# Optimization experiments

Hardware: AMD Instinct MI355X
Metric: run time of the kernel (lower is better)

## Reference

```python
import jax, jax.numpy as jnp
import numpy as np

N_NODES = 19385
N_EDGES = 1_200_000
GNN = 256
HID = 512
RANK = 512
NCLS = 3
NGENES = 6640
NBLK = 6
B = 256
EPS = 1e-5


def _ln(x, g, b):
    m = jnp.mean(x, axis=-1, keepdims=True)
    v = jnp.mean(jnp.square(x - m), axis=-1, keepdims=True)
    return (x - m) * jax.lax.rsqrt(v + EPS) * g + b


def setup_inputs() -> dict:
    key = jax.random.key(0)
    ks = iter(jax.random.split(key, 40))
    w = lambda shape, s=0.02: jax.random.normal(next(ks), shape, jnp.float32) * s
    inp = {
        'node_idx': jax.random.randint(next(ks), (B,), -1, N_NODES),  # -1 == OOV
        'edge_index': jax.random.randint(next(ks), (2, N_EDGES), 0, N_NODES),
        'edge_weight': jax.random.uniform(next(ks), (N_EDGES,), jnp.float32),
        'frozen_emb': jax.random.normal(next(ks), (N_NODES, GNN), jnp.float32),
        # trainable partial GNN (mps.6, mps.7, post_mp)
        'conv6_W': w((GNN, GNN)), 'conv6_b': jnp.zeros((GNN,)),
        'ln6_g': jnp.ones((GNN,)), 'ln6_b': jnp.zeros((GNN,)),
        'conv7_W': w((GNN, GNN)), 'conv7_b': jnp.zeros((GNN,)),
        'ln7_g': jnp.ones((GNN,)), 'ln7_b': jnp.zeros((GNN,)),
        'post_W': w((GNN, GNN)), 'post_b': jnp.zeros((GNN,)),
        # head
        'oov_emb': w((GNN,)),
        'in_ln_g': jnp.ones((GNN,)), 'in_ln_b': jnp.zeros((GNN,)),
        'proj_in_W': w((GNN, HID)), 'proj_in_b': jnp.zeros((HID,)),
        'rb_ln_g': jnp.ones((NBLK, HID)), 'rb_ln_b': jnp.zeros((NBLK, HID)),
        'rb_W1': w((NBLK, HID, 4 * HID)), 'rb_b1': jnp.zeros((NBLK, 4 * HID)),
        'rb_W2': w((NBLK, 4 * HID, HID)), 'rb_b2': jnp.zeros((NBLK, HID)),
        'out_ln_g': jnp.ones((HID,)), 'out_ln_b': jnp.zeros((HID,)),
        'bil_W': w((HID, NCLS * RANK)), 'bil_b': jnp.zeros((NCLS * RANK,)),
        'out_gene_emb': w((NGENES, RANK)),
    }
    return inp


def reference(node_idx, edge_index, edge_weight, frozen_emb,
              conv6_W, conv6_b, ln6_g, ln6_b,
              conv7_W, conv7_b, ln7_g, ln7_b,
              post_W, post_b,
              oov_emb, in_ln_g, in_ln_b, proj_in_W, proj_in_b,
              rb_ln_g, rb_ln_b, rb_W1, rb_b1, rb_W2, rb_b2,
              out_ln_g, out_ln_b, bil_W, bil_b, out_gene_emb):
    src, dst = edge_index[0], edge_index[1]

    def conv(x, W, b):
        # edge-weighted message passing: gather -> scale -> scatter-add -> linear
        msg = x[src] * edge_weight[:, None]              # [E, GNN]
        agg = jax.ops.segment_sum(msg, dst, num_segments=N_NODES)
        return agg @ W + b

    # trainable GNN layers (eval mode: dropout = identity)
    x = frozen_emb
    x = x + jax.nn.relu(_ln(conv(x, conv6_W, conv6_b), ln6_g, ln6_b))
    x = x + jax.nn.relu(_ln(conv(x, conv7_W, conv7_b), ln7_g, ln7_b))
    node_emb = x @ post_W + post_b                       # [N, GNN]

    # OOV-aware lookup
    in_f = (node_idx >= 0).astype(jnp.float32)[:, None]  # [B,1]
    gnn_emb = node_emb[jnp.clip(node_idx, 0, None)]      # [B, GNN]
    h = gnn_emb * in_f + oov_emb[None, :] * (1.0 - in_f)

    # MLP head
    h = _ln(h, in_ln_g, in_ln_b) @ proj_in_W + proj_in_b
    for i in range(NBLK):
        t = _ln(h, rb_ln_g[i], rb_ln_b[i])
        t = jax.nn.gelu(t @ rb_W1[i] + rb_b1[i])
        h = h + t @ rb_W2[i] + rb_b2[i]
    h = _ln(h, out_ln_g, out_ln_b)

    pert = (h @ bil_W + bil_b).reshape(B, NCLS, RANK)
    logits = jnp.einsum('bcr,gr->bcg', pert, out_gene_emb)  # [B, 3, 6640]
    return logits
```

## Files before the change

### kernel.cpp

```cpp
#include <hip/hip_runtime.h>
#include <hip/hip_bf16.h>
#include <cstdint>
#include <cstddef>

#define N_NODES_C 19385
#define N_EDGES_C 1200000
#define GNN_C 256
#define HID_C 512
#define RANK_C 512
#define NCLS_C 3
#define NGENES_C 6640
#define NBLK_C 6
#define B_C 256
#define LN_EPS 1e-5f

#define PH_K 256
#define PH_CHUNK ((N_EDGES_C + PH_K - 1) / PH_K)
#define PH_NW ((N_NODES_C + 1) / 2)

typedef short bf8v __attribute__((ext_vector_type(8)));
typedef float f4v __attribute__((ext_vector_type(4)));
typedef int i2v __attribute__((ext_vector_type(2)));

__device__ __forceinline__ float bfu2f(unsigned short u) {
  union { unsigned int i; float f; } c; c.i = ((unsigned)u) << 16; return c.f;
}
__device__ __forceinline__ unsigned short f2bfu(float v) {
  union { float f; unsigned u; } c; c.f = v;
  unsigned r = c.u + 0x7FFFu + ((c.u >> 16) & 1u);
  return (unsigned short)(r >> 16);
}
__device__ __forceinline__ float gelu_tanh(float v) {
  const float x3 = v * v * v;
  return 0.5f * v * (1.f + tanhf(0.7978845608028654f * (v + 0.044715f * x3)));
}


struct CvtSeg { const float* s; unsigned short* d; long long n; };
struct CvtArgs { CvtSeg seg[2]; int nseg; };

__global__ __launch_bounds__(256) void multicvt_kernel(CvtArgs a) {
  for (int sg = 0; sg < a.nseg; ++sg) {
    const float4* s = reinterpret_cast<const float4*>(a.seg[sg].s);
    unsigned short* d = a.seg[sg].d;
    const long long n4 = a.seg[sg].n >> 2;
    for (long long i = blockIdx.x * 256 + threadIdx.x; i < n4;
         i += (long long)gridDim.x * 256) {
      float4 v = s[i];
      ushort4 o;
      o.x = f2bfu(v.x); o.y = f2bfu(v.y); o.z = f2bfu(v.z); o.w = f2bfu(v.w);
      *reinterpret_cast<ushort4*>(d + i * 4) = o;
    }
  }
}


struct TSeg { const float* s; unsigned short* d; int R, C; };
struct TArgs { TSeg seg[12]; int nseg; };

__global__ __launch_bounds__(256) void multitrans_kernel(TArgs a) {
  __shared__ float tile[32][33];
  const int tx = threadIdx.x & 31;
  const int ty = threadIdx.x >> 5;
  for (int sg = 0; sg < a.nseg; ++sg) {
    const int R = a.seg[sg].R, C = a.seg[sg].C;
    const int tC = C >> 5;
    const int nt = (R >> 5) * tC;
    const float* src = a.seg[sg].s;
    unsigned short* dst = a.seg[sg].d;
    for (int tid = blockIdx.x; tid < nt; tid += gridDim.x) {
      const int tr = tid / tC, tc = tid - tr * tC;
      const int r0 = tr * 32, c0 = tc * 32;
      __syncthreads();
#pragma unroll
      for (int j = 0; j < 32; j += 8)
        tile[ty + j][tx] = src[(size_t)(r0 + ty + j) * C + c0 + tx];
      __syncthreads();
#pragma unroll
      for (int j = 0; j < 32; j += 8)
        dst[(size_t)(c0 + ty + j) * R + r0 + tx] = f2bfu(tile[tx][ty + j]);
    }
  }
}


__global__ __launch_bounds__(256) void marksel_kernel(const int* __restrict__ node_idx,
                                                      int* __restrict__ selbm,
                                                      int* __restrict__ needed) {
  const int b = threadIdx.x;
  const int n = max(node_idx[b], 0);
  selbm[n] = 1;
  needed[n] = 1;
}

__global__ __launch_bounds__(1024) void privhist_kernel(const int* __restrict__ src,
                                                        const int* __restrict__ dst,
                                                        const int* __restrict__ selbm,
                                                        int* __restrict__ needed,
                                                        unsigned int* __restrict__ cntp) {
  __shared__ unsigned int bins[PH_NW];
  const int t = threadIdx.x;
  for (int w = t; w < PH_NW; w += 1024) bins[w] = 0u;
  __syncthreads();
  const int base = blockIdx.x * PH_CHUNK;
  const int end = min(base + PH_CHUNK, N_EDGES_C);
#pragma unroll 2
  for (int i = base + t; i < end; i += 1024) {
    const int d = dst[i];
    atomicAdd(&bins[d >> 1], 1u << ((d & 1) * 16));
    if (selbm[d]) needed[src[i]] = 1;
  }
  __syncthreads();
  unsigned int* out = cntp + (size_t)blockIdx.x * PH_NW;
  for (int w = t; w < PH_NW; w += 1024) out[w] = bins[w];
}

__global__ __launch_bounds__(256) void redhist_kernel(unsigned int* __restrict__ cntp,
                                                      int* __restrict__ cnt) {
  const int w = blockIdx.x * 256 + threadIdx.x;
  if (w >= PH_NW) return;
  unsigned int lo = 0, hi = 0;
#pragma unroll 4
  for (int k = 0; k < PH_K; ++k) {
    const size_t idx = (size_t)k * PH_NW + w;
    const unsigned int u = cntp[idx];
    cntp[idx] = lo | (hi << 16);
    lo += u & 0xFFFFu;
    hi += u >> 16;
  }
  cnt[2 * w] = (int)lo;
  if (2 * w + 1 < N_NODES_C) cnt[2 * w + 1] = (int)hi;
}

__global__ __launch_bounds__(1024) void scan_kernel(const int* __restrict__ cnt,
                                                    int* __restrict__ off, int n) {
  __shared__ int sums[1024];
  const int t = threadIdx.x;
  const int CH = (n + 1023) >> 10;
  const int base = t * CH;
  int s = 0;
  for (int i = 0; i < CH; ++i) {
    int idx = base + i;
    if (idx < n) s += cnt[idx];
  }
  sums[t] = s;
  __syncthreads();
  for (int d = 1; d < 1024; d <<= 1) {
    int v = (t >= d) ? sums[t - d] : 0;
    __syncthreads();
    sums[t] += v;
    __syncthreads();
  }
  int run = (t == 0) ? 0 : sums[t - 1];
  for (int i = 0; i < CH; ++i) {
    int idx = base + i;
    if (idx < n) { off[idx] = run; run += cnt[idx]; }
  }
  if (t == 0) off[n] = sums[1023];
}

__global__ __launch_bounds__(1024) void fill_kernel(const int* __restrict__ src,
                                                    const int* __restrict__ dst,
                                                    const float* __restrict__ ew,
                                                    const int* __restrict__ off,
                                                    const unsigned int* __restrict__ cntp,
                                                    const int* __restrict__ needed,
                                                    i2v* __restrict__ ep) {
  __shared__ unsigned int bins[PH_NW];
  const int t = threadIdx.x;
  const unsigned int* myp = cntp + (size_t)blockIdx.x * PH_NW;
  for (int w = t; w < PH_NW; w += 1024) bins[w] = myp[w];
  __syncthreads();
  const int base = blockIdx.x * PH_CHUNK;
  const int end = min(base + PH_CHUNK, N_EDGES_C);
#pragma unroll 2
  for (int i = base + t; i < end; i += 1024) {
    const int d = dst[i];
    if (!needed[d]) continue;
    const int sh = (d & 1) * 16;
    const unsigned int old = atomicAdd(&bins[d >> 1], 1u << sh);
    const int rank = (int)((old >> sh) & 0xFFFFu);
    i2v e;
    e[0] = src[i] * GNN_C;
    e[1] = __float_as_int(ew[i]);
    ep[off[d] + rank] = e;
  }
}


__global__ __launch_bounds__(256) void agg_full_kernel(const i2v* __restrict__ ep,
                                                       const int* __restrict__ off,
                                                       const int* __restrict__ needed,
                                                       const unsigned short* __restrict__ x,
                                                       unsigned short* __restrict__ aggbf) {
  const int n = blockIdx.x;
  if (!needed[n]) return;
  __shared__ f4v red[4][64];
  const int t = threadIdx.x;
  const int w = __builtin_amdgcn_readfirstlane(t >> 6);
  const int lane = t & 63;
  const int s0 = off[n];
  const int c = off[n + 1] - s0;
  const int q0 = s0 + ((c * w) >> 2);
  const int q1 = s0 + ((c * (w + 1)) >> 2);
  float a0 = 0.f, a1 = 0.f, a2 = 0.f, a3 = 0.f;
  const unsigned short* xl = x + 4 * lane;
#pragma unroll 4
  for (int p = q0; p < q1; ++p) {
    const i2v e = ep[p];
    const int s = e[0];
    const float wg = __int_as_float(e[1]);
    const ushort4 v = *reinterpret_cast<const ushort4*>(xl + s);
    a0 = fmaf(bfu2f(v.x), wg, a0);
    a1 = fmaf(bfu2f(v.y), wg, a1);
    a2 = fmaf(bfu2f(v.z), wg, a2);
    a3 = fmaf(bfu2f(v.w), wg, a3);
  }
  f4v av; av[0] = a0; av[1] = a1; av[2] = a2; av[3] = a3;
  red[w][lane] = av;
  __syncthreads();
  const float* rf = reinterpret_cast<const float*>(red);
  const float sum = rf[t] + rf[256 + t] + rf[512 + t] + rf[768 + t];
  aggbf[(size_t)n * GNN_C + t] = f2bfu(sum);
}

__global__ __launch_bounds__(256) void agg_sel_kernel(const int* __restrict__ node_idx,
                                                      const i2v* __restrict__ ep,
                                                      const int* __restrict__ off,
                                                      const float* __restrict__ x,
                                                      unsigned short* __restrict__ aggbf) {
  __shared__ f4v red[4][64];
  const int b = blockIdx.x;
  const int t = threadIdx.x;
  const int n = max(node_idx[b], 0);
  const int w = __builtin_amdgcn_readfirstlane(t >> 6);
  const int lane = t & 63;
  const int s0 = off[n];
  const int c = off[n + 1] - s0;
  const int q0 = s0 + ((c * w) >> 2);
  const int q1 = s0 + ((c * (w + 1)) >> 2);
  float a0 = 0.f, a1 = 0.f, a2 = 0.f, a3 = 0.f;
  const float* xl = x + 4 * lane;
#pragma unroll 2
  for (int p = q0; p < q1; ++p) {
    const i2v e = ep[p];
    const int s = e[0];
    const float wg = __int_as_float(e[1]);
    const f4v v = *reinterpret_cast<const f4v*>(xl + s);
    a0 = fmaf(v[0], wg, a0);
    a1 = fmaf(v[1], wg, a1);
    a2 = fmaf(v[2], wg, a2);
    a3 = fmaf(v[3], wg, a3);
  }
  f4v av; av[0] = a0; av[1] = a1; av[2] = a2; av[3] = a3;
  red[w][lane] = av;
  __syncthreads();
  const float* rf = reinterpret_cast<const float*>(red);
  const float sum = rf[t] + rf[256 + t] + rf[512 + t] + rf[768 + t];
  aggbf[(size_t)b * GNN_C + t] = f2bfu(sum);
}


#define MBK 32
#define MLDW 40

__global__ __launch_bounds__(256) void mgemm_kernel(const unsigned short* __restrict__ A,
                                                    const unsigned short* __restrict__ Bt,
                                                    const float* __restrict__ bias,
                                                    float* __restrict__ C,
                                                    int M, int N, int K) {
  __shared__ unsigned short As[128][MLDW];
  __shared__ unsigned short Bs[128][MLDW];
  const int t = threadIdx.x;
  const int lane = t & 63;
  const int wave = t >> 6;
  const int r0 = blockIdx.x * 128;
  const int c0 = blockIdx.y * 128;
  const int wm = (wave >> 1) * 64;
  const int wn = (wave & 1) * 64;
  const int lm = lane & 15;
  const int lq = lane >> 4;

  f4v acc[4][4];
  for (int i = 0; i < 4; ++i)
    for (int j = 0; j < 4; ++j)
      for (int r = 0; r < 4; ++r) acc[i][j][r] = 0.f;

  const int row = t >> 1;
  const int kof = (t & 1) * 16;
  for (int k0 = 0; k0 < K; k0 += MBK) {
    {
      const int gr = r0 + row;
      uint4 u0 = make_uint4(0, 0, 0, 0), u1 = u0;
      if (gr < M) {
        const uint4* p = reinterpret_cast<const uint4*>(A + (size_t)gr * K + k0 + kof);
        u0 = p[0]; u1 = p[1];
      }
      *reinterpret_cast<uint4*>(&As[row][kof]) = u0;
      *reinterpret_cast<uint4*>(&As[row][kof + 8]) = u1;
    }
    {
      const int gn = c0 + row;
      uint4 u0 = make_uint4(0, 0, 0, 0), u1 = u0;
      if (gn < N) {
        const uint4* p = reinterpret_cast<const uint4*>(Bt + (size_t)gn * K + k0 + kof);
        u0 = p[0]; u1 = p[1];
      }
      *reinterpret_cast<uint4*>(&Bs[row][kof]) = u0;
      *reinterpret_cast<uint4*>(&Bs[row][kof + 8]) = u1;
    }
    __syncthreads();

    bf8v a[4], b[4];
#pragma unroll
    for (int i = 0; i < 4; ++i)
      a[i] = *reinterpret_cast<const bf8v*>(&As[wm + i * 16 + lm][lq * 8]);
#pragma unroll
    for (int j = 0; j < 4; ++j)
      b[j] = *reinterpret_cast<const bf8v*>(&Bs[wn + j * 16 + lm][lq * 8]);
#pragma unroll
    for (int i = 0; i < 4; ++i)
#pragma unroll
      for (int j = 0; j < 4; ++j)
        acc[i][j] = __builtin_amdgcn_mfma_f32_16x16x32_bf16(a[i], b[j], acc[i][j], 0, 0, 0);
    __syncthreads();
  }

  for (int ti = 0; ti < 4; ++ti) {
    for (int tj = 0; tj < 4; ++tj) {
      const int col = c0 + wn + tj * 16 + lm;
      if (col >= N) continue;
      const float bv = bias ? bias[col] : 0.f;
      for (int r = 0; r < 4; ++r) {
        const int row2 = r0 + wm + ti * 16 + lq * 4 + r;
        if (row2 < M) C[(size_t)row2 * N + col] = acc[ti][tj][r] + bv;
      }
    }
  }
}


__global__ __launch_bounds__(256) void mgemm64_kernel(const unsigned short* __restrict__ A,
                                                      const unsigned short* __restrict__ Bt,
                                                      const float* __restrict__ bias,
                                                      float* outF, unsigned short* outB,
                                                      int M, int N, int K, int doGelu) {
  __shared__ unsigned short As[64][MLDW];
  __shared__ unsigned short Bs[64][MLDW];
  const int t = threadIdx.x;
  const int lane = t & 63;
  const int wave = t >> 6;
  const int r0 = blockIdx.x * 64;
  const int c0 = blockIdx.y * 64;
  const int wm = (wave >> 1) * 32;
  const int wn = (wave & 1) * 32;
  const int lm = lane & 15;
  const int lq = lane >> 4;

  f4v acc[2][2];
  for (int i = 0; i < 2; ++i)
    for (int j = 0; j < 2; ++j)
      for (int r = 0; r < 4; ++r) acc[i][j][r] = 0.f;

  const int row = t >> 2;
  const int kof = (t & 3) * 8;
  for (int k0 = 0; k0 < K; k0 += MBK) {
    *reinterpret_cast<uint4*>(&As[row][kof]) =
        *reinterpret_cast<const uint4*>(A + (size_t)(r0 + row) * K + k0 + kof);
    *reinterpret_cast<uint4*>(&Bs[row][kof]) =
        *reinterpret_cast<const uint4*>(Bt + (size_t)(c0 + row) * K + k0 + kof);
    __syncthreads();
    bf8v a[2], b[2];
#pragma unroll
    for (int i = 0; i < 2; ++i)
      a[i] = *reinterpret_cast<const bf8v*>(&As[wm + i * 16 + lm][lq * 8]);
#pragma unroll
    for (int j = 0; j < 2; ++j)
      b[j] = *reinterpret_cast<const bf8v*>(&Bs[wn + j * 16 + lm][lq * 8]);
#pragma unroll
    for (int i = 0; i < 2; ++i)
#pragma unroll
      for (int j = 0; j < 2; ++j)
        acc[i][j] = __builtin_amdgcn_mfma_f32_16x16x32_bf16(a[i], b[j], acc[i][j], 0, 0, 0);
    __syncthreads();
  }

  for (int ti = 0; ti < 2; ++ti) {
    for (int tj = 0; tj < 2; ++tj) {
      const int col = c0 + wn + tj * 16 + lm;
      const float bv = bias ? bias[col] : 0.f;
      for (int r = 0; r < 4; ++r) {
        const int row2 = r0 + wm + ti * 16 + lq * 4 + r;
        float v = acc[ti][tj][r] + bv;
        if (doGelu) v = gelu_tanh(v);
        if (outF) outF[(size_t)row2 * N + col] = v;
        else outB[(size_t)row2 * N + col] = f2bfu(v);
      }
    }
  }
}

__global__ __launch_bounds__(256) void skmgemm64_kernel(const unsigned short* __restrict__ A,
                                                        const unsigned short* __restrict__ Bt,
                                                        float* __restrict__ part,
                                                        int M, int N, int K, int kc) {
  __shared__ unsigned short As[64][MLDW];
  __shared__ unsigned short Bs[64][MLDW];
  const int t = threadIdx.x;
  const int lane = t & 63;
  const int wave = t >> 6;
  const int r0 = blockIdx.x * 64;
  const int c0 = blockIdx.y * 64;
  const int kBeg = blockIdx.z * kc;
  const int kEnd = kBeg + kc;
  const int wm = (wave >> 1) * 32;
  const int wn = (wave & 1) * 32;
  const int lm = lane & 15;
  const int lq = lane >> 4;

  f4v acc[2][2];
  for (int i = 0; i < 2; ++i)
    for (int j = 0; j < 2; ++j)
      for (int r = 0; r < 4; ++r) acc[i][j][r] = 0.f;

  const int row = t >> 2;
  const int kof = (t & 3) * 8;
  for (int k0 = kBeg; k0 < kEnd; k0 += MBK) {
    *reinterpret_cast<uint4*>(&As[row][kof]) =
        *reinterpret_cast<const uint4*>(A + (size_t)(r0 + row) * K + k0 + kof);
    *reinterpret_cast<uint4*>(&Bs[row][kof]) =
        *reinterpret_cast<const uint4*>(Bt + (size_t)(c0 + row) * K + k0 + kof);
    __syncthreads();
    bf8v a[2], b[2];
#pragma unroll
    for (int i = 0; i < 2; ++i)
      a[i] = *reinterpret_cast<const bf8v*>(&As[wm + i * 16 + lm][lq * 8]);
#pragma unroll
    for (int j = 0; j < 2; ++j)
      b[j] = *reinterpret_cast<const bf8v*>(&Bs[wn + j * 16 + lm][lq * 8]);
#pragma unroll
    for (int i = 0; i < 2; ++i)
#pragma unroll
      for (int j = 0; j < 2; ++j)
        acc[i][j] = __builtin_amdgcn_mfma_f32_16x16x32_bf16(a[i], b[j], acc[i][j], 0, 0, 0);
    __syncthreads();
  }

  float* out = part + (size_t)blockIdx.z * M * N;
  for (int ti = 0; ti < 2; ++ti)
    for (int tj = 0; tj < 2; ++tj) {
      const int col = c0 + wn + tj * 16 + lm;
      for (int r = 0; r < 4; ++r) {
        const int row2 = r0 + wm + ti * 16 + lq * 4 + r;
        out[(size_t)row2 * N + col] = acc[ti][tj][r];
      }
    }
}


__global__ __launch_bounds__(256) void postconv6_kernel(const float* __restrict__ g,
                                                        const float* __restrict__ b,
                                                        const float* __restrict__ frozen,
                                                        const int* __restrict__ needed,
                                                        float* __restrict__ yx) {
  __shared__ float sb[4];
  const int n = blockIdx.x, t = threadIdx.x;
  if (!needed[n]) return;
  const float v = yx[(size_t)n * GNN_C + t];
  float s = v;
  for (int o = 32; o; o >>= 1) s += __shfl_down(s, o, 64);
  if ((t & 63) == 0) sb[t >> 6] = s;
  __syncthreads();
  const float m = (sb[0] + sb[1] + sb[2] + sb[3]) * (1.f / GNN_C);
  __syncthreads();
  const float d = v - m;
  s = d * d;
  for (int o = 32; o; o >>= 1) s += __shfl_down(s, o, 64);
  if ((t & 63) == 0) sb[t >> 6] = s;
  __syncthreads();
  const float rs = rsqrtf((sb[0] + sb[1] + sb[2] + sb[3]) * (1.f / GNN_C) + LN_EPS);
  const float xn = d * rs * g[t] + b[t];
  yx[(size_t)n * GNN_C + t] = frozen[(size_t)n * GNN_C + t] + fmaxf(xn, 0.f);
}

__global__ __launch_bounds__(256) void postconv7_kernel(const float* __restrict__ y,
                                                        const float* __restrict__ g,
                                                        const float* __restrict__ b,
                                                        const int* __restrict__ idx,
                                                        const float* __restrict__ x1f,
                                                        unsigned short* __restrict__ out) {
  __shared__ float sb[4];
  const int bi = blockIdx.x, t = threadIdx.x;
  const int n = max(idx[bi], 0);
  const float v = y[(size_t)bi * GNN_C + t];
  float s = v;
  for (int o = 32; o; o >>= 1) s += __shfl_down(s, o, 64);
  if ((t & 63) == 0) sb[t >> 6] = s;
  __syncthreads();
  const float m = (sb[0] + sb[1] + sb[2] + sb[3]) * (1.f / GNN_C);
  __syncthreads();
  const float d = v - m;
  s = d * d;
  for (int o = 32; o; o >>= 1) s += __shfl_down(s, o, 64);
  if ((t & 63) == 0) sb[t >> 6] = s;
  __syncthreads();
  const float rs = rsqrtf((sb[0] + sb[1] + sb[2] + sb[3]) * (1.f / GNN_C) + LN_EPS);
  const float xn = d * rs * g[t] + b[t];
  out[(size_t)bi * GNN_C + t] = f2bfu(x1f[(size_t)n * GNN_C + t] + fmaxf(xn, 0.f));
}

__global__ __launch_bounds__(256) void h0ln_kernel(const float* __restrict__ ne,
                                                   const int* __restrict__ idx,
                                                   const float* __restrict__ oov,
                                                   const float* __restrict__ g,
                                                   const float* __restrict__ b,
                                                   unsigned short* __restrict__ out) {
  __shared__ float sb[4];
  const int bi = blockIdx.x, t = threadIdx.x;
  const float v = (idx[bi] >= 0) ? ne[(size_t)bi * GNN_C + t] : oov[t];
  float s = v;
  for (int o = 32; o; o >>= 1) s += __shfl_down(s, o, 64);
  if ((t & 63) == 0) sb[t >> 6] = s;
  __syncthreads();
  const float m = (sb[0] + sb[1] + sb[2] + sb[3]) * (1.f / GNN_C);
  __syncthreads();
  const float d = v - m;
  s = d * d;
  for (int o = 32; o; o >>= 1) s += __shfl_down(s, o, 64);
  if ((t & 63) == 0) sb[t >> 6] = s;
  __syncthreads();
  const float rs = rsqrtf((sb[0] + sb[1] + sb[2] + sb[3]) * (1.f / GNN_C) + LN_EPS);
  out[(size_t)bi * GNN_C + t] = f2bfu(d * rs * g[t] + b[t]);
}

__global__ __launch_bounds__(256) void lnbf_kernel(const float* __restrict__ in,
                                                   const float* __restrict__ g,
                                                   const float* __restrict__ b,
                                                   unsigned short* __restrict__ out) {
  __shared__ float sb[4];
  const int r = blockIdx.x, t = threadIdx.x;
  const float v0 = in[(size_t)r * HID_C + t];
  const float v1 = in[(size_t)r * HID_C + t + 256];
  float s = v0 + v1;
  for (int o = 32; o; o >>= 1) s += __shfl_down(s, o, 64);
  if ((t & 63) == 0) sb[t >> 6] = s;
  __syncthreads();
  const float m = (sb[0] + sb[1] + sb[2] + sb[3]) * (1.f / HID_C);
  __syncthreads();
  const float d0 = v0 - m, d1 = v1 - m;
  s = d0 * d0 + d1 * d1;
  for (int o = 32; o; o >>= 1) s += __shfl_down(s, o, 64);
  if ((t & 63) == 0) sb[t >> 6] = s;
  __syncthreads();
  const float rs = rsqrtf((sb[0] + sb[1] + sb[2] + sb[3]) * (1.f / HID_C) + LN_EPS);
  out[(size_t)r * HID_C + t] = f2bfu(d0 * rs * g[t] + b[t]);
  out[(size_t)r * HID_C + t + 256] = f2bfu(d1 * rs * g[t + 256] + b[t + 256]);
}

__global__ __launch_bounds__(256) void combln_kernel(const float* __restrict__ part,
                                                     float* __restrict__ h,
                                                     const float* __restrict__ b2,
                                                     const float* __restrict__ g,
                                                     const float* __restrict__ b,
                                                     unsigned short* __restrict__ out) {
  __shared__ float sb[4];
  const int r = blockIdx.x, t = threadIdx.x;
  const int MN = B_C * HID_C;
  const size_t o0 = (size_t)r * HID_C + t;
  const size_t o1 = o0 + 256;
  float v0 = h[o0] + b2[t] + part[o0] + part[MN + o0] + part[2 * MN + o0] + part[3 * MN + o0];
  float v1 = h[o1] + b2[t + 256] + part[o1] + part[MN + o1] + part[2 * MN + o1] + part[3 * MN + o1];
  h[o0] = v0;
  h[o1] = v1;
  float s = v0 + v1;
  for (int o = 32; o; o >>= 1) s += __shfl_down(s, o, 64);
  if ((t & 63) == 0) sb[t >> 6] = s;
  __syncthreads();
  const float m = (sb[0] + sb[1] + sb[2] + sb[3]) * (1.f / HID_C);
  __syncthreads();
  const float d0 = v0 - m, d1 = v1 - m;
  s = d0 * d0 + d1 * d1;
  for (int o = 32; o; o >>= 1) s += __shfl_down(s, o, 64);
  if ((t & 63) == 0) sb[t >> 6] = s;
  __syncthreads();
  const float rs = rsqrtf((sb[0] + sb[1] + sb[2] + sb[3]) * (1.f / HID_C) + LN_EPS);
  out[o0] = f2bfu(d0 * rs * g[t] + b[t]);
  out[o1] = f2bfu(d1 * rs * g[t + 256] + b[t + 256]);
}


extern "C" void kernel_launch(void* const* d_in, const int* in_sizes, int n_in,
                              void* d_out, int out_size, void* d_ws, size_t ws_size,
                              hipStream_t stream) {
  const int* node_idx = (const int*)d_in[0];
  const int* e_src = (const int*)d_in[1];
  const int* e_dst = e_src + N_EDGES_C;
  const float* ew = (const float*)d_in[2];
  const float* frozen = (const float*)d_in[3];
  const float* W6 = (const float*)d_in[4];
  const float* b6 = (const float*)d_in[5];
  const float* g6 = (const float*)d_in[6];
  const float* bl6 = (const float*)d_in[7];
  const float* W7 = (const float*)d_in[8];
  const float* b7 = (const float*)d_in[9];
  const float* g7 = (const float*)d_in[10];
  const float* bl7 = (const float*)d_in[11];
  const float* postW = (const float*)d_in[12];
  const float* postb = (const float*)d_in[13];
  const float* oov = (const float*)d_in[14];
  const float* ing = (const float*)d_in[15];
  const float* inb = (const float*)d_in[16];
  const float* projW = (const float*)d_in[17];
  const float* projb = (const float*)d_in[18];
  const float* rbg = (const float*)d_in[19];
  const float* rbb = (const float*)d_in[20];
  const float* rbW1 = (const float*)d_in[21];
  const float* rbb1 = (const float*)d_in[22];
  const float* rbW2 = (const float*)d_in[23];
  const float* rbb2 = (const float*)d_in[24];
  const float* outg = (const float*)d_in[25];
  const float* outb = (const float*)d_in[26];
  const float* bilW = (const float*)d_in[27];
  const float* bilb = (const float*)d_in[28];
  const float* gene = (const float*)d_in[29];
  (void)in_sizes; (void)n_in; (void)out_size; (void)ws_size;

  char* ws = (char*)d_ws;
  size_t o = 0;
  auto alloc = [&](size_t bytes) -> char* {
    char* p = ws + o;
    o += (bytes + 255) & ~(size_t)255;
    return p;
  };
  int* cnt = (int*)alloc((size_t)N_NODES_C * 4);
  int* off = (int*)alloc((size_t)(N_NODES_C + 1) * 4);
  int* needed = (int*)alloc((size_t)N_NODES_C * 4);
  int* selbm = (int*)alloc((size_t)N_NODES_C * 4);
  unsigned int* cntp = (unsigned int*)alloc((size_t)PH_K * PH_NW * 4);
  i2v* ep = (i2v*)alloc((size_t)N_EDGES_C * 8);
  unsigned short* frozbf = (unsigned short*)alloc((size_t)N_NODES_C * GNN_C * 2);
  char* aggregion = alloc((size_t)NBLK_C * HID_C * 4 * HID_C * 2);
  unsigned short* w6t = (unsigned short*)alloc((size_t)GNN_C * GNN_C * 2);
  unsigned short* w7t = (unsigned short*)alloc((size_t)GNN_C * GNN_C * 2);
  unsigned short* postWt = (unsigned short*)alloc((size_t)GNN_C * GNN_C * 2);
  unsigned short* projWt = (unsigned short*)alloc((size_t)HID_C * GNN_C * 2);
  unsigned short* bilWt = (unsigned short*)alloc((size_t)NCLS_C * RANK_C * HID_C * 2);
  float* yx = (float*)alloc((size_t)N_NODES_C * GNN_C * 4);
  unsigned short* rbW2t = (unsigned short*)alloc((size_t)NBLK_C * 4 * HID_C * HID_C * 2);
  float* part = (float*)alloc((size_t)4 * B_C * HID_C * 4);
  unsigned short* agg7bf = (unsigned short*)alloc((size_t)B_C * GNN_C * 2);
  float* y7b = (float*)alloc((size_t)B_C * GNN_C * 4);
  unsigned short* x2bf = (unsigned short*)alloc((size_t)B_C * GNN_C * 2);
  float* nemb = (float*)alloc((size_t)B_C * GNN_C * 4);
  unsigned short* h0lbf = (unsigned short*)alloc((size_t)B_C * GNN_C * 2);
  float* h = (float*)alloc((size_t)B_C * HID_C * 4);
  unsigned short* tbf = (unsigned short*)alloc((size_t)B_C * HID_C * 2);
  unsigned short* ubf = (unsigned short*)alloc((size_t)B_C * 4 * HID_C * 2);
  unsigned short* pertbf = (unsigned short*)alloc((size_t)B_C * NCLS_C * RANK_C * 2);

  unsigned short* agg6bf = (unsigned short*)aggregion;
  unsigned short* rbW1t = (unsigned short*)aggregion;
  unsigned short* genebf = frozbf;

  (void)hipMemsetAsync(needed, 0, (size_t)N_NODES_C * 4, stream);
  (void)hipMemsetAsync(selbm, 0, (size_t)N_NODES_C * 4, stream);
  marksel_kernel<<<1, 256, 0, stream>>>(node_idx, selbm, needed);
  privhist_kernel<<<PH_K, 1024, 0, stream>>>(e_src, e_dst, selbm, needed, cntp);
  redhist_kernel<<<(PH_NW + 255) / 256, 256, 0, stream>>>(cntp, cnt);
  scan_kernel<<<1, 1024, 0, stream>>>(cnt, off, N_NODES_C);
  fill_kernel<<<PH_K, 1024, 0, stream>>>(e_src, e_dst, ew, off, cntp, needed, ep);

  {
    CvtArgs a;
    a.seg[0] = {frozen, frozbf, (long long)N_NODES_C * GNN_C};
    a.nseg = 1;
    multicvt_kernel<<<512, 256, 0, stream>>>(a);
  }
  {
    TArgs a;
    a.seg[0] = {W6, w6t, GNN_C, GNN_C};
    a.seg[1] = {W7, w7t, GNN_C, GNN_C};
    a.seg[2] = {postW, postWt, GNN_C, GNN_C};
    a.seg[3] = {projW, projWt, GNN_C, HID_C};
    a.seg[4] = {bilW, bilWt, HID_C, NCLS_C * RANK_C};
    a.nseg = 5;
    multitrans_kernel<<<512, 256, 0, stream>>>(a);
  }

  agg_full_kernel<<<N_NODES_C, 256, 0, stream>>>(ep, off, needed, frozbf, agg6bf);
  {
    dim3 g((N_NODES_C + 127) / 128, GNN_C / 128);
    mgemm_kernel<<<g, 256, 0, stream>>>(agg6bf, w6t, b6, yx, N_NODES_C, GNN_C, GNN_C);
  }
  postconv6_kernel<<<N_NODES_C, 256, 0, stream>>>(g6, bl6, frozen, needed, yx);

  {
    TArgs a;
    for (int i = 0; i < NBLK_C; ++i) {
      a.seg[i] = {rbW1 + (size_t)i * HID_C * 4 * HID_C,
                  rbW1t + (size_t)i * HID_C * 4 * HID_C, HID_C, 4 * HID_C};
      a.seg[6 + i] = {rbW2 + (size_t)i * 4 * HID_C * HID_C,
                      rbW2t + (size_t)i * 4 * HID_C * HID_C, 4 * HID_C, HID_C};
    }
    a.nseg = 12;
    multitrans_kernel<<<2048, 256, 0, stream>>>(a);
  }
  {
    CvtArgs a;
    a.seg[0] = {gene, genebf, (long long)NGENES_C * RANK_C};
    a.nseg = 1;
    multicvt_kernel<<<512, 256, 0, stream>>>(a);
  }

  agg_sel_kernel<<<B_C, 256, 0, stream>>>(node_idx, ep, off, yx, agg7bf);
  {
    dim3 g(B_C / 64, GNN_C / 64);
    mgemm64_kernel<<<g, 256, 0, stream>>>(agg7bf, w7t, b7, y7b, nullptr,
                                          B_C, GNN_C, GNN_C, 0);
  }
  postconv7_kernel<<<B_C, 256, 0, stream>>>(y7b, g7, bl7, node_idx, yx, x2bf);

  {
    dim3 g(B_C / 64, GNN_C / 64);
    mgemm64_kernel<<<g, 256, 0, stream>>>(x2bf, postWt, postb, nemb, nullptr,
                                          B_C, GNN_C, GNN_C, 0);
  }
  h0ln_kernel<<<B_C, 256, 0, stream>>>(nemb, node_idx, oov, ing, inb, h0lbf);

  {
    dim3 g(B_C / 64, HID_C / 64);
    mgemm64_kernel<<<g, 256, 0, stream>>>(h0lbf, projWt, projb, h, nullptr,
                                          B_C, HID_C, GNN_C, 0);
  }
  lnbf_kernel<<<B_C, 256, 0, stream>>>(h, rbg, rbb, tbf);

  for (int i = 0; i < NBLK_C; ++i) {
    {
      dim3 g(B_C / 64, (4 * HID_C) / 64);
      mgemm64_kernel<<<g, 256, 0, stream>>>(tbf, rbW1t + (size_t)i * HID_C * 4 * HID_C,
                                            rbb1 + (size_t)i * 4 * HID_C, nullptr, ubf,
                                            B_C, 4 * HID_C, HID_C, 1);
    }
    {
      dim3 g(B_C / 64, HID_C / 64, 4);
      skmgemm64_kernel<<<g, 256, 0, stream>>>(ubf, rbW2t + (size_t)i * 4 * HID_C * HID_C,
                                              part, B_C, HID_C, 4 * HID_C, HID_C);
    }
    const float* gn = (i < NBLK_C - 1) ? rbg + (size_t)(i + 1) * HID_C : outg;
    const float* bn = (i < NBLK_C - 1) ? rbb + (size_t)(i + 1) * HID_C : outb;
    combln_kernel<<<B_C, 256, 0, stream>>>(part, h, rbb2 + (size_t)i * HID_C, gn, bn, tbf);
  }

  {
    dim3 g(B_C / 64, (NCLS_C * RANK_C) / 64);
    mgemm64_kernel<<<g, 256, 0, stream>>>(tbf, bilWt, bilb, nullptr, pertbf,
                                          B_C, NCLS_C * RANK_C, HID_C, 0);
  }

  {
    dim3 g((B_C * NCLS_C) / 128, (NGENES_C + 127) / 128);
    mgemm_kernel<<<g, 256, 0, stream>>>(pertbf, genebf, nullptr, (float*)d_out,
                                        B_C * NCLS_C, NGENES_C, RANK_C);
  }
}
```

Measured before the change: 585.5 us.

## Fuse conv6 GEMM with LayerNorm/ReLU/residual epilogue and merge init marking

Replaces the separate conv6 GEMM and per-node postconv6 LayerNorm kernel with one kernel. Each 512-thread block computes a full 64-row by 256-column output tile and applies bias, LayerNorm, ReLU and the frozen residual in registers, reducing across waves through shared memory. This removes the intermediate fp32 yx write and reread and one kernel launch. Two memsets plus the single-block mark kernel are also replaced by one kernel that builds both mask arrays by comparing each node against the 256 selected indices. The fused GEMM tile has fewer blocks and a heavier register footprint, and the brute-force marking does 256 comparisons per node.

Result: no change. 594.3 us (+1.5%).

```diff
diff --git a/kernel.cpp b/kernel.cpp
--- a/kernel.cpp
+++ b/kernel.cpp
@@ -84,13 +84,20 @@
 }
 
 
-__global__ __launch_bounds__(256) void marksel_kernel(const int* __restrict__ node_idx,
-                                                      int* __restrict__ selbm,
-                                                      int* __restrict__ needed) {
-  const int b = threadIdx.x;
-  const int n = max(node_idx[b], 0);
-  selbm[n] = 1;
-  needed[n] = 1;
+__global__ __launch_bounds__(256) void initmark_kernel(const int* __restrict__ node_idx,
+                                                       int* __restrict__ selbm,
+                                                       int* __restrict__ needed) {
+  __shared__ int sel[B_C];
+  sel[threadIdx.x] = max(node_idx[threadIdx.x], 0);
+  __syncthreads();
+  for (int i = blockIdx.x * 256 + threadIdx.x; i < N_NODES_C;
+       i += gridDim.x * 256) {
+    int m = 0;
+#pragma unroll 16
+    for (int j = 0; j < B_C; ++j) m |= (sel[j] == i);
+    selbm[i] = m;
+    needed[i] = m;
+  }
 }
 
 __global__ __launch_bounds__(1024) void privhist_kernel(const int* __restrict__ src,
@@ -457,31 +464,124 @@
     }
 }
 
-
-__global__ __launch_bounds__(256) void postconv6_kernel(const float* __restrict__ g,
-                                                        const float* __restrict__ b,
-                                                        const float* __restrict__ frozen,
-                                                        const int* __restrict__ needed,
-                                                        float* __restrict__ yx) {
-  __shared__ float sb[4];
-  const int n = blockIdx.x, t = threadIdx.x;
-  if (!needed[n]) return;
-  const float v = yx[(size_t)n * GNN_C + t];
-  float s = v;
-  for (int o = 32; o; o >>= 1) s += __shfl_down(s, o, 64);
-  if ((t & 63) == 0) sb[t >> 6] = s;
-  __syncthreads();
-  const float m = (sb[0] + sb[1] + sb[2] + sb[3]) * (1.f / GNN_C);
-  __syncthreads();
-  const float d = v - m;
-  s = d * d;
-  for (int o = 32; o; o >>= 1) s += __shfl_down(s, o, 64);
-  if ((t & 63) == 0) sb[t >> 6] = s;
-  __syncthreads();
-  const float rs = rsqrtf((sb[0] + sb[1] + sb[2] + sb[3]) * (1.f / GNN_C) + LN_EPS);
-  const float xn = d * rs * g[t] + b[t];
-  yx[(size_t)n * GNN_C + t] = frozen[(size_t)n * GNN_C + t] + fmaxf(xn, 0.f);
-}
+__global__ __launch_bounds__(512) void gemmln6_kernel(const unsigned short* __restrict__ A,
+                                                      const unsigned short* __restrict__ Bt,
+                                                      const float* __restrict__ bias,
+                                                      const float* __restrict__ g,
+                                                      const float* __restrict__ b,
+                                                      const float* __restrict__ frozen,
+                                                      const int* __restrict__ needed,
+                                                      float* __restrict__ yx, int M) {
+  __shared__ unsigned short As[64][MLDW];
+  __shared__ unsigned short Bs[256][MLDW];
+  __shared__ float rs[64][8];
+  const int t = threadIdx.x;
+  const int lane = t & 63;
+  const int wave = t >> 6;
+  const int r0 = blockIdx.x * 64;
+  const int lm = lane & 15, lq = lane >> 4;
+
+  f4v acc[4][2];
+#pragma unroll
+  for (int i = 0; i < 4; ++i)
+#pragma unroll
+    for (int j = 0; j < 2; ++j)
+#pragma unroll
+      for (int r = 0; r < 4; ++r) acc[i][j][r] = 0.f;
+
+  const int arow = t >> 3, akof = (t & 7) * 4;
+  const int brow = t >> 1, bkof = (t & 1) * 16;
+  for (int k0 = 0; k0 < GNN_C; k0 += MBK) {
+    ushort4 u = make_ushort4(0, 0, 0, 0);
+    const int gr = r0 + arow;
+    if (gr < M) u = *reinterpret_cast<const ushort4*>(A + (size_t)gr * GNN_C + k0 + akof);
+    *reinterpret_cast<ushort4*>(&As[arow][akof]) = u;
+    const uint4* p = reinterpret_cast<const uint4*>(Bt + (size_t)brow * GNN_C + k0 + bkof);
+    *reinterpret_cast<uint4*>(&Bs[brow][bkof]) = p[0];
+    *reinterpret_cast<uint4*>(&Bs[brow][bkof + 8]) = p[1];
+    __syncthreads();
+    bf8v a[4], bf[2];
+#pragma unroll
+    for (int ti = 0; ti < 4; ++ti)
+      a[ti] = *reinterpret_cast<const bf8v*>(&As[ti * 16 + lm][lq * 8]);
+#pragma unroll
+    for (int tj = 0; tj < 2; ++tj)
+      bf[tj] = *reinterpret_cast<const bf8v*>(&Bs[wave * 32 + tj * 16 + lm][lq * 8]);
+#pragma unroll
+    for (int ti = 0; ti < 4; ++ti)
+#pragma unroll
+      for (int tj = 0; tj < 2; ++tj)
+        acc[ti][tj] = __builtin_amdgcn_mfma_f32_16x16x32_bf16(a[ti], bf[tj], acc[ti][tj], 0, 0, 0);
+    __syncthreads();
+  }
+
+  const int c0 = wave * 32 + lm, c1 = c0 + 16;
+  const float b0 = bias[c0], b1 = bias[c1];
+#pragma unroll
+  for (int ti = 0; ti < 4; ++ti)
+#pragma unroll
+    for (int r = 0; r < 4; ++r) { acc[ti][0][r] += b0; acc[ti][1][r] += b1; }
+
+  float m[4][4];
+#pragma unroll
+  for (int ti = 0; ti < 4; ++ti)
+#pragma unroll
+    for (int r = 0; r < 4; ++r) {
+      float s = acc[ti][0][r] + acc[ti][1][r];
+      for (int o = 1; o < 16; o <<= 1) s += __shfl_xor(s, o, 64);
+      if (lm == 0) rs[ti * 16 + lq * 4 + r][wave] = s;
+    }
+  __syncthreads();
+#pragma unroll
+  for (int ti = 0; ti < 4; ++ti)
+#pragma unroll
+    for (int r = 0; r < 4; ++r) {
+      const int row = ti * 16 + lq * 4 + r;
+      float s = 0.f;
+#pragma unroll
+      for (int w2 = 0; w2 < 8; ++w2) s += rs[row][w2];
+      m[ti][r] = s * (1.f / GNN_C);
+    }
+  __syncthreads();
+  float iv[4][4];
+#pragma unroll
+  for (int ti = 0; ti < 4; ++ti)
+#pragma unroll
+    for (int r = 0; r < 4; ++r) {
+      const float d0 = acc[ti][0][r] - m[ti][r];
+      const float d1 = acc[ti][1][r] - m[ti][r];
+      float s = d0 * d0 + d1 * d1;
+      for (int o = 1; o < 16; o <<= 1) s += __shfl_xor(s, o, 64);
+      if (lm == 0) rs[ti * 16 + lq * 4 + r][wave] = s;
+    }
+  __syncthreads();
+#pragma unroll
+  for (int ti = 0; ti < 4; ++ti)
+#pragma unroll
+    for (int r = 0; r < 4; ++r) {
+      const int row = ti * 16 + lq * 4 + r;
+      float s = 0.f;
+#pragma unroll
+      for (int w2 = 0; w2 < 8; ++w2) s += rs[row][w2];
+      iv[ti][r] = rsqrtf(s * (1.f / GNN_C) + LN_EPS);
+    }
+
+  const float g0 = g[c0], g1 = g[c1], bb0 = b[c0], bb1 = b[c1];
+#pragma unroll
+  for (int ti = 0; ti < 4; ++ti)
+#pragma unroll
+    for (int r = 0; r < 4; ++r) {
+      const int grow = r0 + ti * 16 + lq * 4 + r;
+      if (grow < M && needed[grow]) {
+        const size_t base = (size_t)grow * GNN_C;
+        const float x0 = fmaxf((acc[ti][0][r] - m[ti][r]) * iv[ti][r] * g0 + bb0, 0.f);
+        const float x1 = fmaxf((acc[ti][1][r] - m[ti][r]) * iv[ti][r] * g1 + bb1, 0.f);
+        yx[base + c0] = frozen[base + c0] + x0;
+        yx[base + c1] = frozen[base + c1] + x1;
+      }
+    }
+}
+
 
 __global__ __launch_bounds__(256) void postconv7_kernel(const float* __restrict__ y,
                                                         const float* __restrict__ g,
@@ -583,9 +683,9 @@
   for (int o = 32; o; o >>= 1) s += __shfl_down(s, o, 64);
   if ((t & 63) == 0) sb[t >> 6] = s;
   __syncthreads();
-  const float rs = rsqrtf((sb[0] + sb[1] + sb[2] + sb[3]) * (1.f / HID_C) + LN_EPS);
-  out[o0] = f2bfu(d0 * rs * g[t] + b[t]);
-  out[o1] = f2bfu(d1 * rs * g[t + 256] + b[t + 256]);
+  const float rsq = rsqrtf((sb[0] + sb[1] + sb[2] + sb[3]) * (1.f / HID_C) + LN_EPS);
+  out[o0] = f2bfu(d0 * rsq * g[t] + b[t]);
+  out[o1] = f2bfu(d1 * rsq * g[t + 256] + b[t + 256]);
 }
 
 
@@ -662,9 +762,7 @@
   unsigned short* rbW1t = (unsigned short*)aggregion;
   unsigned short* genebf = frozbf;
 
-  (void)hipMemsetAsync(needed, 0, (size_t)N_NODES_C * 4, stream);
-  (void)hipMemsetAsync(selbm, 0, (size_t)N_NODES_C * 4, stream);
-  marksel_kernel<<<1, 256, 0, stream>>>(node_idx, selbm, needed);
+  initmark_kernel<<<80, 256, 0, stream>>>(node_idx, selbm, needed);
   privhist_kernel<<<PH_K, 1024, 0, stream>>>(e_src, e_dst, selbm, needed, cntp);
   redhist_kernel<<<(PH_NW + 255) / 256, 256, 0, stream>>>(cntp, cnt);
   scan_kernel<<<1, 1024, 0, stream>>>(cnt, off, N_NODES_C);
@@ -688,11 +786,8 @@
   }
 
   agg_full_kernel<<<N_NODES_C, 256, 0, stream>>>(ep, off, needed, frozbf, agg6bf);
-  {
-    dim3 g((N_NODES_C + 127) / 128, GNN_C / 128);
-    mgemm_kernel<<<g, 256, 0, stream>>>(agg6bf, w6t, b6, yx, N_NODES_C, GNN_C, GNN_C);
-  }
-  postconv6_kernel<<<N_NODES_C, 256, 0, stream>>>(g6, bl6, frozen, needed, yx);
+  gemmln6_kernel<<<(N_NODES_C + 63) / 64, 512, 0, stream>>>(agg6bf, w6t, b6, g6, bl6,
+                                                            frozen, needed, yx, N_NODES_C);
 
   {
     TArgs a;
```
